# Optimization experiments

Hardware: AMD Instinct MI355X
Metric: run time of the kernel (lower is better)

## Reference

```python
import jax, jax.numpy as jnp
import numpy as np

L, H, D, FF = 6, 16, 768, 3072
B, N = 4, 1023
HD = D // H  # 48
EPS = 1e-5


def _layernorm(x, w, b):
    m = jnp.mean(x, axis=-1, keepdims=True)
    v = jnp.mean((x - m) ** 2, axis=-1, keepdims=True)
    return (x - m) / jnp.sqrt(v + EPS) * w + b


def setup_inputs() -> dict:
    key = jax.random.key(0)
    ks = jax.random.split(key, 10)
    ratio = 2.0 ** (-8.0 / H)
    slopes = np.array([ratio ** (i + 1) for i in range(H)], dtype=np.float32)
    return {
        "cls_tokens": jax.random.normal(ks[0], (B, N, D), jnp.float32),
        "cls_token": jax.random.normal(ks[1], (1, 1, D), jnp.float32) * 0.02,
        "log_slopes": jnp.log(jnp.asarray(slopes)),
        "Wqkv": jax.random.normal(ks[2], (L, 3 * D, D), jnp.float32) * 0.02,
        "Wo": jax.random.normal(ks[3], (L, D, D), jnp.float32) * 0.02,
        "Wg": jax.random.normal(ks[4], (L, FF, D), jnp.float32) * 0.02,
        "Wu": jax.random.normal(ks[5], (L, FF, D), jnp.float32) * 0.02,
        "Wd": jax.random.normal(ks[6], (L, D, FF), jnp.float32) * 0.02,
        "ln1_w": jnp.ones((L, D), jnp.float32),
        "ln1_b": jnp.zeros((L, D), jnp.float32),
        "ln2_w": jnp.ones((L, D), jnp.float32),
        "ln2_b": jnp.zeros((L, D), jnp.float32),
        "fin_w": jnp.ones((D,), jnp.float32),
        "fin_b": jnp.zeros((D,), jnp.float32),
    }


def reference(cls_tokens, cls_token, log_slopes, Wqkv, Wo, Wg, Wu, Wd,
              ln1_w, ln1_b, ln2_w, ln2_b, fin_w, fin_b):
    b, n, dmodel = cls_tokens.shape
    S = n + 1
    # learnable ALiBi: -exp(log_slope) * |i - j|, shape (H, S, S)
    pos = jnp.arange(S)
    dist = jnp.abs(pos[None, :] - pos[:, None]).astype(cls_tokens.dtype)
    bias = -(jnp.exp(log_slopes)[:, None, None] * dist[None, :, :])

    x = jnp.concatenate([jnp.broadcast_to(cls_token, (b, 1, dmodel)), cls_tokens], axis=1)
    scale = 1.0 / jnp.sqrt(jnp.asarray(HD, x.dtype))

    for l in range(L):
        h = _layernorm(x, ln1_w[l], ln1_b[l])
        qkv = jnp.einsum('bsd,ed->bse', h, Wqkv[l]).reshape(b, S, 3, H, HD)
        qkv = qkv.transpose(2, 0, 3, 1, 4)  # (3, B, H, S, hd)
        q, k, v = qkv[0], qkv[1], qkv[2]
        scores = jnp.einsum('bhqd,bhkd->bhqk', q, k) * scale + bias[None]
        attn = jax.nn.softmax(scores, axis=-1)
        o = jnp.einsum('bhqk,bhkd->bhqd', attn, v)
        o = o.transpose(0, 2, 1, 3).reshape(b, S, dmodel)
        x = x + jnp.einsum('bsd,ed->bse', o, Wo[l])
        h = _layernorm(x, ln2_w[l], ln2_b[l])
        gate = jax.nn.silu(jnp.einsum('bsd,fd->bsf', h, Wg[l]))
        up = jnp.einsum('bsd,fd->bsf', h, Wu[l])
        x = x + jnp.einsum('bsf,df->bsd', gate * up, Wd[l])

    return _layernorm(x[:, 0, :], fin_w, fin_b)
```

## Files before the change

kernel.cpp:

```cpp
#include <hip/hip_runtime.h>
#include <hip/hip_bf16.h>

#define LNUM 6
#define HNUM 16
#define DMODEL 768
#define FFDIM 3072
#define BATCH 4
#define NTOK 1023
#define SEQ 1024
#define HD 48
#define EPS 1e-5f

typedef __hip_bfloat16 bf16;

__device__ __forceinline__ unsigned short f2bf_raw(float f) {
  bf16 h = __float2bfloat16(f);
  union { bf16 h; unsigned short s; } u; u.h = h; return u.s;
}
__device__ __forceinline__ float bflo(unsigned int u) { return __uint_as_float(u << 16); }
__device__ __forceinline__ float bfhi(unsigned int u) { return __uint_as_float(u & 0xffff0000u); }

__global__ __launch_bounds__(256) void concat_kernel(
    const float* __restrict__ cls_tokens, const float* __restrict__ cls_token,
    float* __restrict__ x) {
  size_t i = (size_t)blockIdx.x * blockDim.x + threadIdx.x;
  const size_t total = (size_t)BATCH * SEQ * DMODEL;
  if (i >= total) return;
  int d = (int)(i % DMODEL);
  size_t bs = i / DMODEL;
  int s = (int)(bs % SEQ);
  int b = (int)(bs / SEQ);
  float v;
  if (s == 0) v = cls_token[d];
  else v = cls_tokens[((size_t)b * NTOK + (s - 1)) * DMODEL + d];
  x[i] = v;
}

#define W_QKV4  442368
#define W_O4    147456
#define W_FF4   589824
__global__ __launch_bounds__(256) void convert_w_kernel(
    const float* __restrict__ wqkv, const float* __restrict__ wo,
    const float* __restrict__ wg, const float* __restrict__ wu,
    const float* __restrict__ wd, bf16* __restrict__ dst) {
  size_t i4 = (size_t)blockIdx.x * 256 + threadIdx.x;
  size_t off4 = i4;
  const float* src;
  if (off4 < W_QKV4) src = wqkv;
  else { off4 -= W_QKV4;
    if (off4 < W_O4) src = wo;
    else { off4 -= W_O4;
      if (off4 < W_FF4) src = wg;
      else { off4 -= W_FF4;
        if (off4 < W_FF4) src = wu;
        else { off4 -= W_FF4; src = wd; } } } }
  float4 v = ((const float4*)src)[off4];
  ushort4 o;
  o.x = f2bf_raw(v.x); o.y = f2bf_raw(v.y);
  o.z = f2bf_raw(v.z); o.w = f2bf_raw(v.w);
  ((ushort4*)dst)[i4] = o;
}

__device__ __forceinline__ void st_ln(float* p, float v) { *p = v; }
__device__ __forceinline__ void st_ln(bf16* p, float v) { *p = __float2bfloat16(v); }

template <typename OUT>
__global__ __launch_bounds__(256) void ln_kernel(
    const float* __restrict__ in, OUT* __restrict__ out,
    const float* __restrict__ w, const float* __restrict__ bias,
    size_t in_stride, size_t out_stride) {
  const int row = blockIdx.x;
  const int tid = threadIdx.x;
  const float* x = in + (size_t)row * in_stride;
  OUT* y = out + (size_t)row * out_stride;

  float v0 = x[tid], v1 = x[tid + 256], v2 = x[tid + 512];
  float s = v0 + v1 + v2;
  float sq = v0 * v0 + v1 * v1 + v2 * v2;

  __shared__ float s_sum[256];
  __shared__ float s_sq[256];
  s_sum[tid] = s;
  s_sq[tid] = sq;
  __syncthreads();
  for (int off = 128; off > 0; off >>= 1) {
    if (tid < off) {
      s_sum[tid] += s_sum[tid + off];
      s_sq[tid] += s_sq[tid + off];
    }
    __syncthreads();
  }
  const float inv_d = 1.0f / (float)DMODEL;
  float mean = s_sum[0] * inv_d;
  float var = s_sq[0] * inv_d - mean * mean;
  float rstd = rsqrtf(var + EPS);

  st_ln(y + tid,       (v0 - mean) * rstd * w[tid]       + bias[tid]);
  st_ln(y + tid + 256, (v1 - mean) * rstd * w[tid + 256] + bias[tid + 256]);
  st_ln(y + tid + 512, (v2 - mean) * rstd * w[tid + 512] + bias[tid + 512]);
}

#define BM 128
#define BN 128
#define BK 32

typedef __attribute__((ext_vector_type(8))) short bfrag;
typedef __attribute__((ext_vector_type(4))) float f32x4;

__device__ __forceinline__ void async_copy16(const void* g, void* l) {
  __builtin_amdgcn_global_load_lds(
      (const __attribute__((address_space(1))) void*)g,
      (__attribute__((address_space(3))) void*)l, 16, 0, 0);
}

template <int CMODE>
__global__ __launch_bounds__(256) void gemm_bf16(
    const bf16* __restrict__ A, const bf16* __restrict__ B,
    void* __restrict__ Cv, int M, int N, int K) {
  __shared__ bf16 As[BM][BK];
  __shared__ bf16 Bs[BN][BK];

  const int tid = threadIdx.x;
  const int wave = tid >> 6;
  const int lane = tid & 63;
  const int m0 = blockIdx.y * BM;
  const int n0 = blockIdx.x * BN;
  const int wm = (wave & 1) * 64;
  const int wn = (wave >> 1) * 64;

  f32x4 acc[4][4];
#pragma unroll
  for (int i = 0; i < 4; i++)
#pragma unroll
    for (int j = 0; j < 4; j++) acc[i][j] = (f32x4)(0.f);

  const int lrow = lane >> 2;
  const int lcol = (lane & 3) * 8;
  const bf16* Ag[2]; const bf16* Bg[2];
  void *AsB[2], *BsB[2];
#pragma unroll
  for (int j = 0; j < 2; j++) {
    int c = j * 4 + wave;
    Ag[j] = A + (size_t)(m0 + c * 16 + lrow) * K + lcol;
    Bg[j] = B + (size_t)(n0 + c * 16 + lrow) * K + lcol;
    AsB[j] = (void*)&As[c * 16][0];
    BsB[j] = (void*)&Bs[c * 16][0];
  }

  const int fr = lane & 15;
  const int fk = (lane >> 4) * 8;

  for (int k0 = 0; k0 < K; k0 += BK) {
    async_copy16(Ag[0] + k0, AsB[0]);
    async_copy16(Ag[1] + k0, AsB[1]);
    async_copy16(Bg[0] + k0, BsB[0]);
    async_copy16(Bg[1] + k0, BsB[1]);
    __syncthreads();

    bfrag a[4], b[4];
#pragma unroll
    for (int i = 0; i < 4; i++) {
      a[i] = *(const bfrag*)&As[wm + i * 16 + fr][fk];
      b[i] = *(const bfrag*)&Bs[wn + i * 16 + fr][fk];
    }
#pragma unroll
    for (int i = 0; i < 4; i++)
#pragma unroll
      for (int j = 0; j < 4; j++)
        acc[i][j] = __builtin_amdgcn_mfma_f32_16x16x32_bf16(a[i], b[j], acc[i][j], 0, 0, 0);
    __syncthreads();
  }

  const int ccol = lane & 15;
  const int crow = (lane >> 4) * 4;
#pragma unroll
  for (int i = 0; i < 4; i++) {
#pragma unroll
    for (int j = 0; j < 4; j++) {
#pragma unroll
      for (int r = 0; r < 4; r++) {
        const size_t gm = m0 + wm + i * 16 + crow + r;
        const size_t gn = n0 + wn + j * 16 + ccol;
        if (CMODE == 2) {
          ((bf16*)Cv)[gm * N + gn] = __float2bfloat16(acc[i][j][r]);
        } else if (CMODE == 1) {
          float* cp = (float*)Cv + gm * N + gn;
          *cp += acc[i][j][r];
        } else {
          ((float*)Cv)[gm * N + gn] = acc[i][j][r];
        }
      }
    }
  }
}

#define AQT 64
#define AKT 64
#define ASTR 72

__global__ __launch_bounds__(256, 4) void attn_mfma(
    const bf16* __restrict__ qkv, const float* __restrict__ log_slopes,
    bf16* __restrict__ obuf) {
  __shared__ bf16 Qs[AQT][ASTR];
  __shared__ bf16 Ks[AKT][ASTR];
  __shared__ bf16 Vt[HD][ASTR];
  __shared__ bf16 Pt[AQT][ASTR];

  const int tid = threadIdx.x;
  const int wq = tid >> 6;
  const int lane = tid & 63;
  const int l15 = lane & 15;
  const int lh = lane >> 4;
  const int qb = blockIdx.x * AQT;
  const int h = blockIdx.y;
  const int b = blockIdx.z;

  const float scale = 0.14433756729740643f;
  const float slope = __expf(log_slopes[h]);
  const size_t rstride = 3 * DMODEL;
  const bf16* qbase = qkv + ((size_t)(b * SEQ + qb)) * rstride + h * HD;

  for (int it = tid; it < AQT * 2; it += 256) {
    int r = it >> 1, c = it & 1;
    *(uint4*)&Qs[r][48 + c * 8] = make_uint4(0, 0, 0, 0);
    *(uint4*)&Ks[r][48 + c * 8] = make_uint4(0, 0, 0, 0);
  }
  for (int it = tid; it < AQT * 6; it += 256) {
    int r = it / 6, c = it % 6;
    *(uint4*)&Qs[r][c * 8] = *(const uint4*)(qbase + (size_t)r * rstride + c * 8);
  }

  float m[4], l[4];
  f32x4 accO[3];
#pragma unroll
  for (int r = 0; r < 4; r++) { m[r] = -1e30f; l[r] = 0.f; }
#pragma unroll
  for (int t = 0; t < 3; t++) accO[t] = (f32x4)(0.f);

  for (int kb = 0; kb < SEQ; kb += AKT) {
    __syncthreads();
    const bf16* kbase = qkv + ((size_t)(b * SEQ + kb)) * rstride + DMODEL + h * HD;
    for (int it = tid; it < AKT * 6; it += 256) {
      int r = it / 6, c = it % 6;
      *(uint4*)&Ks[r][c * 8] = *(const uint4*)(kbase + (size_t)r * rstride + c * 8);
    }
    if (tid < 192) {
      int p = tid & 31, c = tid >> 5;
      const bf16* v0 = kbase + DMODEL + (size_t)(2 * p) * rstride + c * 8;
      uint4 r0 = *(const uint4*)v0;
      uint4 r1 = *(const uint4*)(v0 + rstride);
      const unsigned int* w0 = (const unsigned int*)&r0;
      const unsigned int* w1 = (const unsigned int*)&r1;
#pragma unroll
      for (int i = 0; i < 8; i++) {
        unsigned int lo = (i & 1) ? (w0[i >> 1] >> 16) : (w0[i >> 1] & 0xffffu);
        unsigned int hi = (i & 1) ? (w1[i >> 1] >> 16) : (w1[i >> 1] & 0xffffu);
        *(unsigned int*)&Vt[c * 8 + i][2 * p] = lo | (hi << 16);
      }
    }
    __syncthreads();

    f32x4 accS[4];
#pragma unroll
    for (int j = 0; j < 4; j++) accS[j] = (f32x4)(0.f);
#pragma unroll
    for (int ks = 0; ks < 2; ks++) {
      bfrag a = *(const bfrag*)&Qs[wq * 16 + l15][ks * 32 + lh * 8];
#pragma unroll
      for (int j = 0; j < 4; j++) {
        bfrag bk = *(const bfrag*)&Ks[j * 16 + l15][ks * 32 + lh * 8];
        accS[j] = __builtin_amdgcn_mfma_f32_16x16x32_bf16(a, bk, accS[j], 0, 0, 0);
      }
    }

    float ps[4][4];
#pragma unroll
    for (int r = 0; r < 4; r++) {
      const int qg = qb + wq * 16 + lh * 4 + r;
      float s[4];
#pragma unroll
      for (int j = 0; j < 4; j++) {
        const int kg = kb + j * 16 + l15;
        s[j] = accS[j][r] * scale - slope * fabsf((float)(qg - kg));
      }
      float mx = fmaxf(fmaxf(s[0], s[1]), fmaxf(s[2], s[3]));
#pragma unroll
      for (int off = 1; off < 16; off <<= 1) mx = fmaxf(mx, __shfl_xor(mx, off, 64));
      const float mnew = fmaxf(m[r], mx);
      const float corr = __expf(m[r] - mnew);
      float rs = 0.f;
#pragma unroll
      for (int j = 0; j < 4; j++) {
        ps[j][r] = __expf(s[j] - mnew);
        rs += ps[j][r];
      }
#pragma unroll
      for (int off = 1; off < 16; off <<= 1) rs += __shfl_xor(rs, off, 64);
      l[r] = l[r] * corr + rs;
      m[r] = mnew;
#pragma unroll
      for (int t = 0; t < 3; t++) accO[t][r] *= corr;
    }

#pragma unroll
    for (int j = 0; j < 4; j++)
#pragma unroll
      for (int r = 0; r < 4; r++)
        Pt[wq * 16 + lh * 4 + r][j * 16 + l15] = __float2bfloat16(ps[j][r]);

#pragma unroll
    for (int ks = 0; ks < 2; ks++) {
      bfrag pa = *(const bfrag*)&Pt[wq * 16 + l15][ks * 32 + lh * 8];
#pragma unroll
      for (int t = 0; t < 3; t++) {
        bfrag vb = *(const bfrag*)&Vt[t * 16 + l15][ks * 32 + lh * 8];
        accO[t] = __builtin_amdgcn_mfma_f32_16x16x32_bf16(pa, vb, accO[t], 0, 0, 0);
      }
    }
  }

#pragma unroll
  for (int r = 0; r < 4; r++) {
    const float inv = 1.0f / l[r];
    bf16* op = obuf + ((size_t)(b * SEQ + qb + wq * 16 + lh * 4 + r)) * DMODEL + h * HD;
#pragma unroll
    for (int t = 0; t < 3; t++)
      op[t * 16 + l15] = __float2bfloat16(accO[t][r] * inv);
  }
}

__global__ __launch_bounds__(256) void silu_mul_kernel(
    bf16* __restrict__ g, const bf16* __restrict__ u, size_t n2) {
  size_t i = (size_t)blockIdx.x * blockDim.x + threadIdx.x;
  size_t stride = (size_t)gridDim.x * blockDim.x;
  unsigned int* gp = (unsigned int*)g;
  const unsigned int* up = (const unsigned int*)u;
  for (; i < n2; i += stride) {
    unsigned int gu_ = gp[i], uu = up[i];
    float g0 = bflo(gu_), g1 = bfhi(gu_);
    float u0 = bflo(uu), u1 = bfhi(uu);
    float r0 = g0 / (1.0f + __expf(-g0)) * u0;
    float r1 = g1 / (1.0f + __expf(-g1)) * u1;
    gp[i] = (unsigned int)f2bf_raw(r0) | ((unsigned int)f2bf_raw(r1) << 16);
  }
}

extern "C" void kernel_launch(void* const* d_in, const int* in_sizes, int n_in,
                              void* d_out, int out_size, void* d_ws, size_t ws_size,
                              hipStream_t stream) {
  const float* cls_tokens = (const float*)d_in[0];
  const float* cls_token  = (const float*)d_in[1];
  const float* log_slopes = (const float*)d_in[2];
  const float* Wqkv = (const float*)d_in[3];
  const float* Wo   = (const float*)d_in[4];
  const float* Wg   = (const float*)d_in[5];
  const float* Wu   = (const float*)d_in[6];
  const float* Wd   = (const float*)d_in[7];
  const float* ln1_w = (const float*)d_in[8];
  const float* ln1_b = (const float*)d_in[9];
  const float* ln2_w = (const float*)d_in[10];
  const float* ln2_b = (const float*)d_in[11];
  const float* fin_w = (const float*)d_in[12];
  const float* fin_b = (const float*)d_in[13];
  float* out = (float*)d_out;

  const size_t ROWS = (size_t)BATCH * SEQ;
  char* wsb = (char*)d_ws;
  float* x    = (float*)(wsb);
  bf16* qkvb  = (bf16*)(wsb + 12582912);
  bf16* hb    = (bf16*)(wsb + 31457280);
  bf16* ob    = (bf16*)(wsb + 37748736);
  bf16* gb    = (bf16*)(wsb + 44040192);
  bf16* ub    = (bf16*)(wsb + 69206016);
  bf16* wbf   = (bf16*)(wsb + 94371840);

  bf16* wqkv_b = wbf;
  bf16* wo_b   = wbf + 1769472;
  bf16* wg_b   = wbf + 2359296;
  bf16* wu_b   = wbf + 4718592;
  bf16* wd_b   = wbf + 7077888;

  {
    const size_t total = ROWS * DMODEL;
    concat_kernel<<<(int)((total + 255) / 256), 256, 0, stream>>>(cls_tokens, cls_token, x);
  }

  for (int l = 0; l < LNUM; l++) {
    convert_w_kernel<<<9216, 256, 0, stream>>>(
        Wqkv + (size_t)l * 3 * DMODEL * DMODEL, Wo + (size_t)l * DMODEL * DMODEL,
        Wg + (size_t)l * FFDIM * DMODEL, Wu + (size_t)l * FFDIM * DMODEL,
        Wd + (size_t)l * DMODEL * FFDIM, wbf);

    ln_kernel<bf16><<<(int)ROWS, 256, 0, stream>>>(
        x, hb, ln1_w + l * DMODEL, ln1_b + l * DMODEL, DMODEL, DMODEL);
    gemm_bf16<2><<<dim3(3 * DMODEL / BN, ROWS / BM), 256, 0, stream>>>(
        hb, wqkv_b, qkvb, (int)ROWS, 3 * DMODEL, DMODEL);
    attn_mfma<<<dim3(SEQ / AQT, HNUM, BATCH), 256, 0, stream>>>(qkvb, log_slopes, ob);
    gemm_bf16<1><<<dim3(DMODEL / BN, ROWS / BM), 256, 0, stream>>>(
        ob, wo_b, x, (int)ROWS, DMODEL, DMODEL);
    ln_kernel<bf16><<<(int)ROWS, 256, 0, stream>>>(
        x, hb, ln2_w + l * DMODEL, ln2_b + l * DMODEL, DMODEL, DMODEL);
    gemm_bf16<2><<<dim3(FFDIM / BN, ROWS / BM), 256, 0, stream>>>(
        hb, wg_b, gb, (int)ROWS, FFDIM, DMODEL);
    gemm_bf16<2><<<dim3(FFDIM / BN, ROWS / BM), 256, 0, stream>>>(
        hb, wu_b, ub, (int)ROWS, FFDIM, DMODEL);
    silu_mul_kernel<<<4096, 256, 0, stream>>>(gb, ub, ROWS * FFDIM / 2);
    gemm_bf16<1><<<dim3(DMODEL / BN, ROWS / BM), 256, 0, stream>>>(
        gb, wd_b, x, (int)ROWS, DMODEL, FFDIM);
  }

  ln_kernel<float><<<BATCH, 256, 0, stream>>>(x, out, fin_w, fin_b,
                                              (size_t)SEQ * DMODEL, DMODEL);
}
```

Baseline: 2.051 ms.

## Double-buffer GEMM LDS tiles and fuse gate/up GEMMs with SiLU epilogue

```diff
diff --git a/kernel.cpp b/kernel.cpp
--- a/kernel.cpp
+++ b/kernel.cpp
@@ -117,8 +117,8 @@
 __global__ __launch_bounds__(256) void gemm_bf16(
     const bf16* __restrict__ A, const bf16* __restrict__ B,
     void* __restrict__ Cv, int M, int N, int K) {
-  __shared__ bf16 As[BM][BK];
-  __shared__ bf16 Bs[BN][BK];
+  __shared__ bf16 As[2][BM][BK];
+  __shared__ bf16 Bs[2][BN][BK];
 
   const int tid = threadIdx.x;
   const int wave = tid >> 6;
@@ -137,38 +137,51 @@
   const int lrow = lane >> 2;
   const int lcol = (lane & 3) * 8;
   const bf16* Ag[2]; const bf16* Bg[2];
-  void *AsB[2], *BsB[2];
+  void *AsB[2][2], *BsB[2][2];
 #pragma unroll
   for (int j = 0; j < 2; j++) {
     int c = j * 4 + wave;
     Ag[j] = A + (size_t)(m0 + c * 16 + lrow) * K + lcol;
     Bg[j] = B + (size_t)(n0 + c * 16 + lrow) * K + lcol;
-    AsB[j] = (void*)&As[c * 16][0];
-    BsB[j] = (void*)&Bs[c * 16][0];
+#pragma unroll
+    for (int bf = 0; bf < 2; bf++) {
+      AsB[bf][j] = (void*)&As[bf][c * 16][0];
+      BsB[bf][j] = (void*)&Bs[bf][c * 16][0];
+    }
+  }
+
+#pragma unroll
+  for (int j = 0; j < 2; j++) {
+    async_copy16(Ag[j], AsB[0][j]);
+    async_copy16(Bg[j], BsB[0][j]);
   }
 
   const int fr = lane & 15;
   const int fk = (lane >> 4) * 8;
-
-  for (int k0 = 0; k0 < K; k0 += BK) {
-    async_copy16(Ag[0] + k0, AsB[0]);
-    async_copy16(Ag[1] + k0, AsB[1]);
-    async_copy16(Bg[0] + k0, BsB[0]);
-    async_copy16(Bg[1] + k0, BsB[1]);
+  const int nk = K / BK;
+
+  for (int ki = 0; ki < nk; ki++) {
+    const int cur = ki & 1;
     __syncthreads();
-
+    if (ki + 1 < nk) {
+      const int k0 = (ki + 1) * BK;
+#pragma unroll
+      for (int j = 0; j < 2; j++) {
+        async_copy16(Ag[j] + k0, AsB[cur ^ 1][j]);
+        async_copy16(Bg[j] + k0, BsB[cur ^ 1][j]);
+      }
+    }
     bfrag a[4], b[4];
 #pragma unroll
     for (int i = 0; i < 4; i++) {
-      a[i] = *(const bfrag*)&As[wm + i * 16 + fr][fk];
-      b[i] = *(const bfrag*)&Bs[wn + i * 16 + fr][fk];
+      a[i] = *(const bfrag*)&As[cur][wm + i * 16 + fr][fk];
+      b[i] = *(const bfrag*)&Bs[cur][wn + i * 16 + fr][fk];
     }
 #pragma unroll
     for (int i = 0; i < 4; i++)
 #pragma unroll
       for (int j = 0; j < 4; j++)
         acc[i][j] = __builtin_amdgcn_mfma_f32_16x16x32_bf16(a[i], b[j], acc[i][j], 0, 0, 0);
-    __syncthreads();
   }
 
   const int ccol = lane & 15;
@@ -194,6 +207,103 @@
   }
 }
 
+__global__ __launch_bounds__(256) void gemm_gateup(
+    const bf16* __restrict__ A, const bf16* __restrict__ Wg,
+    const bf16* __restrict__ Wu, bf16* __restrict__ gu, int M, int N, int K) {
+  __shared__ bf16 As[2][BM][BK];
+  __shared__ bf16 Gs[2][BN][BK];
+  __shared__ bf16 Us[2][BN][BK];
+
+  const int tid = threadIdx.x;
+  const int wave = tid >> 6;
+  const int lane = tid & 63;
+  const int m0 = blockIdx.y * BM;
+  const int n0 = blockIdx.x * BN;
+  const int wm = (wave & 1) * 64;
+  const int wn = (wave >> 1) * 64;
+
+  f32x4 accG[4][4], accU[4][4];
+#pragma unroll
+  for (int i = 0; i < 4; i++)
+#pragma unroll
+    for (int j = 0; j < 4; j++) { accG[i][j] = (f32x4)(0.f); accU[i][j] = (f32x4)(0.f); }
+
+  const int lrow = lane >> 2;
+  const int lcol = (lane & 3) * 8;
+  const bf16 *Ag[2], *Gg[2], *Ug[2];
+  void *AsB[2][2], *GsB[2][2], *UsB[2][2];
+#pragma unroll
+  for (int j = 0; j < 2; j++) {
+    int c = j * 4 + wave;
+    Ag[j] = A + (size_t)(m0 + c * 16 + lrow) * K + lcol;
+    Gg[j] = Wg + (size_t)(n0 + c * 16 + lrow) * K + lcol;
+    Ug[j] = Wu + (size_t)(n0 + c * 16 + lrow) * K + lcol;
+#pragma unroll
+    for (int bf = 0; bf < 2; bf++) {
+      AsB[bf][j] = (void*)&As[bf][c * 16][0];
+      GsB[bf][j] = (void*)&Gs[bf][c * 16][0];
+      UsB[bf][j] = (void*)&Us[bf][c * 16][0];
+    }
+  }
+
+#pragma unroll
+  for (int j = 0; j < 2; j++) {
+    async_copy16(Ag[j], AsB[0][j]);
+    async_copy16(Gg[j], GsB[0][j]);
+    async_copy16(Ug[j], UsB[0][j]);
+  }
+
+  const int fr = lane & 15;
+  const int fk = (lane >> 4) * 8;
+  const int nk = K / BK;
+
+  for (int ki = 0; ki < nk; ki++) {
+    const int cur = ki & 1;
+    __syncthreads();
+    if (ki + 1 < nk) {
+      const int k0 = (ki + 1) * BK;
+#pragma unroll
+      for (int j = 0; j < 2; j++) {
+        async_copy16(Ag[j] + k0, AsB[cur ^ 1][j]);
+        async_copy16(Gg[j] + k0, GsB[cur ^ 1][j]);
+        async_copy16(Ug[j] + k0, UsB[cur ^ 1][j]);
+      }
+    }
+    bfrag a[4], g[4], u[4];
+#pragma unroll
+    for (int i = 0; i < 4; i++) {
+      a[i] = *(const bfrag*)&As[cur][wm + i * 16 + fr][fk];
+      g[i] = *(const bfrag*)&Gs[cur][wn + i * 16 + fr][fk];
+      u[i] = *(const bfrag*)&Us[cur][wn + i * 16 + fr][fk];
+    }
+#pragma unroll
+    for (int i = 0; i < 4; i++)
+#pragma unroll
+      for (int j = 0; j < 4; j++) {
+        accG[i][j] = __builtin_amdgcn_mfma_f32_16x16x32_bf16(a[i], g[j], accG[i][j], 0, 0, 0);
+        accU[i][j] = __builtin_amdgcn_mfma_f32_16x16x32_bf16(a[i], u[j], accU[i][j], 0, 0, 0);
+      }
+  }
+
+  const int ccol = lane & 15;
+  const int crow = (lane >> 4) * 4;
+#pragma unroll
+  for (int i = 0; i < 4; i++) {
+#pragma unroll
+    for (int j = 0; j < 4; j++) {
+#pragma unroll
+      for (int r = 0; r < 4; r++) {
+        const size_t gm = m0 + wm + i * 16 + crow + r;
+        const size_t gn = n0 + wn + j * 16 + ccol;
+        const float gv = accG[i][j][r];
+        const float uv = accU[i][j][r];
+        const float res = gv / (1.0f + __expf(-gv)) * uv;
+        gu[gm * N + gn] = __float2bfloat16(res);
+      }
+    }
+  }
+}
+
 #define AQT 64
 #define AKT 64
 #define ASTR 72
@@ -326,22 +436,6 @@
 #pragma unroll
     for (int t = 0; t < 3; t++)
       op[t * 16 + l15] = __float2bfloat16(accO[t][r] * inv);
-  }
-}
-
-__global__ __launch_bounds__(256) void silu_mul_kernel(
-    bf16* __restrict__ g, const bf16* __restrict__ u, size_t n2) {
-  size_t i = (size_t)blockIdx.x * blockDim.x + threadIdx.x;
-  size_t stride = (size_t)gridDim.x * blockDim.x;
-  unsigned int* gp = (unsigned int*)g;
-  const unsigned int* up = (const unsigned int*)u;
-  for (; i < n2; i += stride) {
-    unsigned int gu_ = gp[i], uu = up[i];
-    float g0 = bflo(gu_), g1 = bfhi(gu_);
-    float u0 = bflo(uu), u1 = bfhi(uu);
-    float r0 = g0 / (1.0f + __expf(-g0)) * u0;
-    float r1 = g1 / (1.0f + __expf(-g1)) * u1;
-    gp[i] = (unsigned int)f2bf_raw(r0) | ((unsigned int)f2bf_raw(r1) << 16);
   }
 }
 
@@ -370,8 +464,7 @@
   bf16* qkvb  = (bf16*)(wsb + 12582912);
   bf16* hb    = (bf16*)(wsb + 31457280);
   bf16* ob    = (bf16*)(wsb + 37748736);
-  bf16* gb    = (bf16*)(wsb + 44040192);
-  bf16* ub    = (bf16*)(wsb + 69206016);
+  bf16* gub   = (bf16*)(wsb + 44040192);
   bf16* wbf   = (bf16*)(wsb + 94371840);
 
   bf16* wqkv_b = wbf;
@@ -400,13 +493,10 @@
         ob, wo_b, x, (int)ROWS, DMODEL, DMODEL);
     ln_kernel<bf16><<<(int)ROWS, 256, 0, stream>>>(
         x, hb, ln2_w + l * DMODEL, ln2_b + l * DMODEL, DMODEL, DMODEL);
-    gemm_bf16<2><<<dim3(FFDIM / BN, ROWS / BM), 256, 0, stream>>>(
-        hb, wg_b, gb, (int)ROWS, FFDIM, DMODEL);
-    gemm_bf16<2><<<dim3(FFDIM / BN, ROWS / BM), 256, 0, stream>>>(
-        hb, wu_b, ub, (int)ROWS, FFDIM, DMODEL);
-    silu_mul_kernel<<<4096, 256, 0, stream>>>(gb, ub, ROWS * FFDIM / 2);
+    gemm_gateup<<<dim3(FFDIM / BN, ROWS / BM), 256, 0, stream>>>(
+        hb, wg_b, wu_b, gub, (int)ROWS, FFDIM, DMODEL);
     gemm_bf16<1><<<dim3(DMODEL / BN, ROWS / BM), 256, 0, stream>>>(
-        gb, wd_b, x, (int)ROWS, DMODEL, FFDIM);
+        gub, wd_b, x, (int)ROWS, DMODEL, FFDIM);
   }
 
   ln_kernel<float><<<BATCH, 256, 0, stream>>>(x, out, fin_w, fin_b,
```

Measured after the change: 1.886 ms. -8.1%, faster.
